# Kernel optimization log

Hardware: AMD Instinct MI355X
Metric: run time of the kernel (lower is better)

Reference implementation:

```python
import jax, jax.numpy as jnp
import numpy as np

NUM_HEADS = 16


def setup_inputs() -> dict:
    k0 = jax.random.key(0)
    ks = jax.random.split(k0, 5)
    T, S, N, E = 1024, 1024, 8, 1024
    query = jax.random.normal(ks[0], (T, N, E), dtype=jnp.float32)
    key_t = jax.random.normal(ks[1], (S, N, E), dtype=jnp.float32)
    value = jax.random.normal(ks[2], (S, N, E), dtype=jnp.float32)
    # xavier-uniform-like scale for in_proj (fan_in=fan_out-ish): gain*sqrt(6/(3E+E))
    lim_in = float(np.sqrt(6.0 / (3 * E + E)))
    in_proj_weight = jax.random.uniform(ks[3], (3 * E, E), dtype=jnp.float32, minval=-lim_in, maxval=lim_in)
    in_proj_bias = jnp.zeros((3 * E,), dtype=jnp.float32)
    lim_out = float(np.sqrt(1.0 / E))
    out_proj_weight = jax.random.uniform(ks[4], (E, E), dtype=jnp.float32, minval=-lim_out, maxval=lim_out)
    out_proj_bias = jnp.zeros((E,), dtype=jnp.float32)
    return {
        'query': query, 'key': key_t, 'value': value,
        'in_proj_weight': in_proj_weight, 'in_proj_bias': in_proj_bias,
        'out_proj_weight': out_proj_weight, 'out_proj_bias': out_proj_bias,
    }


def reference(query, key, value, in_proj_weight, in_proj_bias, out_proj_weight, out_proj_bias):
    # Faithful to the source: q,k,v ALL come from `query` via the 3E in-projection
    # (the torch code projects only `query` and chunks; key/value tensors unused).
    T, N, E = query.shape
    S = key.shape[0]  # must equal T for the reshape, as in the torch code
    H = NUM_HEADS
    D = E // H
    qkv = jnp.einsum('tne,fe->tnf', query, in_proj_weight) + in_proj_bias  # (T,N,3E)
    q, k, v = jnp.split(qkv, 3, axis=-1)
    q = q * (float(D) ** -0.5)
    # (T, N*H, D) -> (N*H, T, D)
    q = q.reshape(T, N * H, D).transpose(1, 0, 2)
    k = k.reshape(S, N * H, D).transpose(1, 0, 2)
    v = v.reshape(S, N * H, D).transpose(1, 0, 2)
    attn = jnp.einsum('btd,bsd->bts', q, k)          # (N*H, T, S)
    attn = jax.nn.softmax(attn, axis=-1)
    out = jnp.einsum('bts,bsd->btd', attn, v)        # (N*H, T, D)
    out = out.transpose(1, 0, 2).reshape(T, N, E)
    out = jnp.einsum('tne,fe->tnf', out, out_proj_weight) + out_proj_bias
    avg_weights = attn.reshape(N, H, T, S).mean(axis=1)  # (N, T, S)
    return out, avg_weights
```

## Files before the change

kernel.cpp:

```cpp
#include <hip/hip_runtime.h>


typedef __bf16 bf16x8 __attribute__((ext_vector_type(8)));
typedef float f32x4 __attribute__((ext_vector_type(4)));
typedef unsigned int u32;
typedef const __attribute__((address_space(1))) u32 gu32;
typedef __attribute__((address_space(3))) u32 lu32;

#define MFMA(a, b, c) __builtin_amdgcn_mfma_f32_16x16x32_bf16((a), (b), (c), 0, 0, 0)

#if __has_builtin(__builtin_amdgcn_exp2f)
#define EXP2(x) __builtin_amdgcn_exp2f(x)
#else
#define EXP2(x) exp2f(x)
#endif

__device__ __forceinline__ unsigned short f2bf(float x) {
    union { float f; unsigned u; } v; v.f = x;
    unsigned r = v.u + 0x7fffu + ((v.u >> 16) & 1u);
    return (unsigned short)(r >> 16);
}

__device__ __forceinline__ bf16x8 frag_ld(const unsigned short* p) {
    return __builtin_bit_cast(bf16x8, *(const uint4*)p);
}

template<int ROWS>
__device__ __forceinline__ void stageNx64(const unsigned short* g, int gs,
                                          unsigned short* lds, int wave, int lane) {
#pragma unroll
    for (int it = 0; it < ROWS / 32; it++) {
        int chunk = wave * (ROWS / 32) + it;
        int row = chunk * 8 + (lane >> 3);
        int cb = (lane & 7) ^ (row & 7);
        const unsigned short* gp = g + (size_t)row * gs + cb * 8;
        unsigned short* lp = lds + chunk * 512;
        __builtin_amdgcn_global_load_lds((gu32*)gp, (lu32*)lp, 16, 0, 0);
    }
}

__device__ __forceinline__ bf16x8 frag_sw(const unsigned short* lds, int row, int cb) {
    return frag_ld(lds + row * 64 + ((cb ^ (row & 7)) << 3));
}

__global__ void k_convert_all(const float* __restrict__ q, const float* __restrict__ wi,
                              const float* __restrict__ wo,
                              unsigned short* __restrict__ xq, unsigned short* __restrict__ xwi,
                              unsigned short* __restrict__ xwo) {
    int i = blockIdx.x * 256 + threadIdx.x;
    const float* src; unsigned short* dst; int off;
    if (i < 2097152)      { src = q;  dst = xq;  off = i; }
    else if (i < 2883584) { src = wi; dst = xwi; off = i - 2097152; }
    else                  { src = wo; dst = xwo; off = i - 2883584; }
    float4 v = ((const float4*)src)[off];
    ushort4 o;
    o.x = f2bf(v.x); o.y = f2bf(v.y); o.z = f2bf(v.z); o.w = f2bf(v.w);
    ((ushort4*)dst)[off] = o;
}

__global__ __launch_bounds__(256) void k_inproj(
    const unsigned short* __restrict__ A, const unsigned short* __restrict__ B,
    const float* __restrict__ bias,
    unsigned short* __restrict__ qbf, unsigned short* __restrict__ kbf,
    unsigned short* __restrict__ vTbf)
{
    __shared__ unsigned short As[128 * 64];
    __shared__ unsigned short Bs[128 * 64];
    const int tid = threadIdx.x;
    const int wave = tid >> 6, lane = tid & 63;
    const int quad = lane >> 4, l16 = lane & 15;
    const int wm = wave >> 1, wn = wave & 1;
    const int m0 = blockIdx.x * 128, n0 = blockIdx.y * 128;

    f32x4 acc[4][4];
#pragma unroll
    for (int i = 0; i < 4; i++)
#pragma unroll
        for (int j = 0; j < 4; j++) acc[i][j] = (f32x4){0.f, 0.f, 0.f, 0.f};

    for (int kt = 0; kt < 1024; kt += 64) {
        __syncthreads();
        stageNx64<128>(A + (size_t)m0 * 1024 + kt, 1024, As, wave, lane);
        stageNx64<128>(B + (size_t)n0 * 1024 + kt, 1024, Bs, wave, lane);
        __syncthreads();
#pragma unroll
        for (int kc = 0; kc < 2; kc++) {
            bf16x8 af[4], bfr[4];
#pragma unroll
            for (int i = 0; i < 4; i++) af[i]  = frag_sw(As, wm * 64 + i * 16 + l16, kc * 4 + quad);
#pragma unroll
            for (int j = 0; j < 4; j++) bfr[j] = frag_sw(Bs, wn * 64 + j * 16 + l16, kc * 4 + quad);
#pragma unroll
            for (int i = 0; i < 4; i++)
#pragma unroll
                for (int j = 0; j < 4; j++) acc[i][j] = MFMA(af[i], bfr[j], acc[i][j]);
        }
    }
    const float QSCALE = 0.125f * 1.4426950408889634f;
    const int c = n0 >> 10;
#pragma unroll
    for (int i = 0; i < 4; i++) {
#pragma unroll
        for (int j = 0; j < 4; j++) {
            int col = n0 + wn * 64 + j * 16 + l16;
            float bv = bias[col];
            int hd = col & 1023, h = hd >> 6, d = hd & 63;
#pragma unroll
            for (int r = 0; r < 4; r++) {
                int row = m0 + wm * 64 + i * 16 + quad * 4 + r;
                int t = row >> 3, n = row & 7;
                int b = n * 16 + h;
                float val = acc[i][j][r] + bv;
                if (c == 0)      qbf[(size_t)b * 65536 + t * 64 + d] = f2bf(val * QSCALE);
                else if (c == 1) kbf[(size_t)b * 65536 + t * 64 + d] = f2bf(val);
                else             vTbf[(size_t)b * 65536 + (size_t)d * 1024 + t] = f2bf(val);
            }
        }
    }
}

__global__ __launch_bounds__(256) void k_pv(
    const unsigned short* __restrict__ qbf, const unsigned short* __restrict__ kbf,
    const unsigned short* __restrict__ vTbf,
    float* __restrict__ il_g, unsigned short* __restrict__ Obf)
{
    __shared__ unsigned short Ks[64 * 64];
    __shared__ unsigned short Vs[64 * 64];
    __shared__ unsigned short Ps[128 * 64];
    const int tid = threadIdx.x;
    const int wave = tid >> 6, lane = tid & 63, quad = lane >> 4, l16 = lane & 15;
    const int blk = blockIdx.x;
    const int xcd = blk & 7, idx = blk >> 3;
    const int b = xcd * 16 + (idx >> 3);
    const int t0 = (idx & 7) * 128;
    const int n = b >> 4, h = b & 15;
    const size_t bb = (size_t)b * 65536;

    bf16x8 aq[2][2];
#pragma unroll
    for (int rf = 0; rf < 2; rf++)
#pragma unroll
        for (int kh = 0; kh < 2; kh++)
            aq[rf][kh] = frag_ld(&qbf[bb + (size_t)(t0 + wave * 32 + rf * 16 + l16) * 64 + kh * 32 + quad * 8]);

    float lsum[2][4];
    f32x4 o[2][4];
#pragma unroll
    for (int rf = 0; rf < 2; rf++)
#pragma unroll
        for (int r = 0; r < 4; r++) lsum[rf][r] = 0.f;
#pragma unroll
    for (int rf = 0; rf < 2; rf++)
#pragma unroll
        for (int df = 0; df < 4; df++) o[rf][df] = (f32x4){0.f, 0.f, 0.f, 0.f};

    for (int st = 0; st < 16; st++) {
        __syncthreads();
        stageNx64<64>(kbf + bb + (size_t)(st * 64) * 64, 64, Ks, wave, lane);
        stageNx64<64>(vTbf + bb + st * 64, 1024, Vs, wave, lane);
        __syncthreads();
#pragma unroll
        for (int cf = 0; cf < 4; cf++) {
            bf16x8 k0 = frag_sw(Ks, cf * 16 + l16, quad);
            bf16x8 k1 = frag_sw(Ks, cf * 16 + l16, 4 + quad);
#pragma unroll
            for (int rf = 0; rf < 2; rf++) {
                f32x4 z = (f32x4){0.f, 0.f, 0.f, 0.f};
                z = MFMA(aq[rf][0], k0, z);
                z = MFMA(aq[rf][1], k1, z);
#pragma unroll
                for (int r = 0; r < 4; r++) {
                    float p = EXP2(z[r]);
                    lsum[rf][r] += p;
                    int prow = wave * 32 + rf * 16 + quad * 4 + r;
                    int col = cf * 16 + l16;
                    Ps[prow * 64 + (((col >> 3) ^ (prow & 7)) << 3) + (col & 7)] = f2bf(p);
                }
            }
        }
#pragma unroll
        for (int kc = 0; kc < 2; kc++) {
            bf16x8 ap0 = frag_sw(Ps, wave * 32 + l16, kc * 4 + quad);
            bf16x8 ap1 = frag_sw(Ps, wave * 32 + 16 + l16, kc * 4 + quad);
#pragma unroll
            for (int df = 0; df < 4; df++) {
                bf16x8 bv = frag_sw(Vs, df * 16 + l16, kc * 4 + quad);
                o[0][df] = MFMA(ap0, bv, o[0][df]);
                o[1][df] = MFMA(ap1, bv, o[1][df]);
            }
        }
    }
#pragma unroll
    for (int rf = 0; rf < 2; rf++)
#pragma unroll
        for (int r = 0; r < 4; r++) {
            float s = lsum[rf][r];
            s += __shfl_xor(s, 1); s += __shfl_xor(s, 2);
            s += __shfl_xor(s, 4); s += __shfl_xor(s, 8);
            lsum[rf][r] = 1.0f / s;
        }
#pragma unroll
    for (int rf = 0; rf < 2; rf++)
#pragma unroll
        for (int df = 0; df < 4; df++)
#pragma unroll
            for (int r = 0; r < 4; r++) {
                int t = t0 + wave * 32 + rf * 16 + quad * 4 + r;
                Obf[(size_t)(t * 8 + n) * 1024 + h * 64 + df * 16 + l16] = f2bf(o[rf][df][r] * lsum[rf][r]);
            }
    if (l16 == 0) {
#pragma unroll
        for (int rf = 0; rf < 2; rf++)
#pragma unroll
            for (int r = 0; r < 4; r++)
                il_g[(size_t)b * 1024 + t0 + wave * 32 + rf * 16 + quad * 4 + r] = lsum[rf][r];
    }
}

__global__ __launch_bounds__(256) void k_avg(
    const unsigned short* __restrict__ qbf, const unsigned short* __restrict__ kbf,
    const float* __restrict__ il_g, float* __restrict__ avg)
{
    __shared__ unsigned short Qs[128 * 64];
    __shared__ unsigned short Ks[128 * 64];
    __shared__ float Is[16 * 128];
    const int tid = threadIdx.x;
    const int wave = tid >> 6, lane = tid & 63, quad = lane >> 4, l16 = lane & 15;
    const int wm = wave >> 1, wn = wave & 1;
    const int blk = blockIdx.x;
    const int n = blk & 7, idx = blk >> 3;
    const int s0 = (idx & 7) * 128, t0 = (idx >> 3) * 128;

    for (int i2 = tid; i2 < 2048; i2 += 256)
        Is[i2] = il_g[(size_t)(n * 16 + (i2 >> 7)) * 1024 + t0 + (i2 & 127)];

    f32x4 acc[4][4];
#pragma unroll
    for (int i = 0; i < 4; i++)
#pragma unroll
        for (int j = 0; j < 4; j++) acc[i][j] = (f32x4){0.f, 0.f, 0.f, 0.f};

    for (int h = 0; h < 16; h++) {
        const size_t bb = (size_t)(n * 16 + h) * 65536;
        __syncthreads();
        stageNx64<128>(qbf + bb + (size_t)t0 * 64, 64, Qs, wave, lane);
        stageNx64<128>(kbf + bb + (size_t)s0 * 64, 64, Ks, wave, lane);
        __syncthreads();
        bf16x8 af[4][2];
        float ir[4][4];
#pragma unroll
        for (int i = 0; i < 4; i++) {
            af[i][0] = frag_sw(Qs, wm * 64 + i * 16 + l16, quad);
            af[i][1] = frag_sw(Qs, wm * 64 + i * 16 + l16, 4 + quad);
#pragma unroll
            for (int r = 0; r < 4; r++) ir[i][r] = Is[h * 128 + wm * 64 + i * 16 + quad * 4 + r];
        }
#pragma unroll
        for (int j = 0; j < 4; j++) {
            bf16x8 b0 = frag_sw(Ks, wn * 64 + j * 16 + l16, quad);
            bf16x8 b1 = frag_sw(Ks, wn * 64 + j * 16 + l16, 4 + quad);
#pragma unroll
            for (int i = 0; i < 4; i++) {
                f32x4 z = (f32x4){0.f, 0.f, 0.f, 0.f};
                z = MFMA(af[i][0], b0, z);
                z = MFMA(af[i][1], b1, z);
#pragma unroll
                for (int r = 0; r < 4; r++)
                    acc[i][j][r] += EXP2(z[r]) * ir[i][r];
            }
        }
    }
#pragma unroll
    for (int i = 0; i < 4; i++)
#pragma unroll
        for (int j = 0; j < 4; j++)
#pragma unroll
            for (int r = 0; r < 4; r++) {
                int t = t0 + wm * 64 + i * 16 + quad * 4 + r;
                int s = s0 + wn * 64 + j * 16 + l16;
                avg[(size_t)n * 1048576 + (size_t)t * 1024 + s] = acc[i][j][r] * 0.0625f;
            }
}

__global__ __launch_bounds__(256) void k_outproj(
    const unsigned short* __restrict__ A, const unsigned short* __restrict__ B,
    const float* __restrict__ bias, float* __restrict__ out)
{
    __shared__ unsigned short As[128 * 64];
    __shared__ unsigned short Bs[128 * 64];
    const int tid = threadIdx.x;
    const int wave = tid >> 6, lane = tid & 63;
    const int quad = lane >> 4, l16 = lane & 15;
    const int wm = wave >> 1, wn = wave & 1;
    const int m0 = blockIdx.x * 128, n0 = blockIdx.y * 128;

    f32x4 acc[4][4];
#pragma unroll
    for (int i = 0; i < 4; i++)
#pragma unroll
        for (int j = 0; j < 4; j++) acc[i][j] = (f32x4){0.f, 0.f, 0.f, 0.f};

    for (int kt = 0; kt < 1024; kt += 64) {
        __syncthreads();
        stageNx64<128>(A + (size_t)m0 * 1024 + kt, 1024, As, wave, lane);
        stageNx64<128>(B + (size_t)n0 * 1024 + kt, 1024, Bs, wave, lane);
        __syncthreads();
#pragma unroll
        for (int kc = 0; kc < 2; kc++) {
            bf16x8 af[4], bfr[4];
#pragma unroll
            for (int i = 0; i < 4; i++) af[i]  = frag_sw(As, wm * 64 + i * 16 + l16, kc * 4 + quad);
#pragma unroll
            for (int j = 0; j < 4; j++) bfr[j] = frag_sw(Bs, wn * 64 + j * 16 + l16, kc * 4 + quad);
#pragma unroll
            for (int i = 0; i < 4; i++)
#pragma unroll
                for (int j = 0; j < 4; j++) acc[i][j] = MFMA(af[i], bfr[j], acc[i][j]);
        }
    }
#pragma unroll
    for (int i = 0; i < 4; i++)
#pragma unroll
        for (int j = 0; j < 4; j++) {
            int col = n0 + wn * 64 + j * 16 + l16;
            float bv = bias[col];
#pragma unroll
            for (int r = 0; r < 4; r++) {
                int row = m0 + wm * 64 + i * 16 + quad * 4 + r;
                out[(size_t)row * 1024 + col] = acc[i][j][r] + bv;
            }
        }
}

extern "C" void kernel_launch(void* const* d_in, const int* in_sizes, int n_in,
                              void* d_out, int out_size, void* d_ws, size_t ws_size,
                              hipStream_t stream)
{
    const float* query = (const float*)d_in[0];
    const float* w_in  = (const float*)d_in[3];
    const float* b_in  = (const float*)d_in[4];
    const float* w_out = (const float*)d_in[5];
    const float* b_out = (const float*)d_in[6];
    float* out = (float*)d_out;
    float* avg = out + 8388608;

    if (ws_size < ((size_t)73 << 20)) return;

    char* ws = (char*)d_ws;
    unsigned short* qbf  = (unsigned short*)(ws);
    unsigned short* kbf  = (unsigned short*)(ws + ((size_t)16 << 20));
    unsigned short* vTbf = (unsigned short*)(ws + ((size_t)32 << 20));
    unsigned short* xbf  = (unsigned short*)(ws + ((size_t)48 << 20));
    unsigned short* wibf = (unsigned short*)(ws + ((size_t)64 << 20));
    unsigned short* wobf = (unsigned short*)(ws + ((size_t)70 << 20));
    float* il_g = (float*)(ws + ((size_t)72 << 20));

    k_convert_all<<<12288, 256, 0, stream>>>(query, w_in, w_out, xbf, wibf, wobf);
    k_inproj<<<dim3(64, 24), 256, 0, stream>>>(xbf, wibf, b_in, qbf, kbf, vTbf);
    k_pv    <<<1024, 256, 0, stream>>>(qbf, kbf, vTbf, il_g, xbf);
    k_avg   <<<512, 256, 0, stream>>>(qbf, kbf, il_g, avg);
    k_outproj<<<dim3(64, 8), 256, 0, stream>>>(xbf, wobf, b_out, out);
}
```

Measured before the change: 357.4 us.

## Double-buffer LDS tiles in projection, PV and averaged-weight kernels

All four tiled kernels now hold two LDS buffers per operand. Each iteration starts staging the next tile while computing on the current one, and only one barrier remains per iteration instead of two. The aim is to hide global-to-LDS load latency behind the MFMA and exp work. The cost is double the LDS per block, which may lower occupancy, particularly for the 64KB GEMM and averaged-weight kernels.

```diff
diff --git a/kernel.cpp b/kernel.cpp
--- a/kernel.cpp
+++ b/kernel.cpp
@@ -64,13 +64,15 @@
     unsigned short* __restrict__ qbf, unsigned short* __restrict__ kbf,
     unsigned short* __restrict__ vTbf)
 {
-    __shared__ unsigned short As[128 * 64];
-    __shared__ unsigned short Bs[128 * 64];
+    __shared__ unsigned short As[2][128 * 64];
+    __shared__ unsigned short Bs[2][128 * 64];
     const int tid = threadIdx.x;
     const int wave = tid >> 6, lane = tid & 63;
     const int quad = lane >> 4, l16 = lane & 15;
     const int wm = wave >> 1, wn = wave & 1;
     const int m0 = blockIdx.x * 128, n0 = blockIdx.y * 128;
+    const unsigned short* Ab = A + (size_t)m0 * 1024;
+    const unsigned short* Bb = B + (size_t)n0 * 1024;
 
     f32x4 acc[4][4];
 #pragma unroll
@@ -78,23 +80,28 @@
 #pragma unroll
         for (int j = 0; j < 4; j++) acc[i][j] = (f32x4){0.f, 0.f, 0.f, 0.f};
 
-    for (int kt = 0; kt < 1024; kt += 64) {
-        __syncthreads();
-        stageNx64<128>(A + (size_t)m0 * 1024 + kt, 1024, As, wave, lane);
-        stageNx64<128>(B + (size_t)n0 * 1024 + kt, 1024, Bs, wave, lane);
-        __syncthreads();
+    stageNx64<128>(Ab, 1024, As[0], wave, lane);
+    stageNx64<128>(Bb, 1024, Bs[0], wave, lane);
+    __syncthreads();
+    for (int it = 0; it < 16; it++) {
+        const int cur = it & 1;
+        if (it < 15) {
+            stageNx64<128>(Ab + (it + 1) * 64, 1024, As[cur ^ 1], wave, lane);
+            stageNx64<128>(Bb + (it + 1) * 64, 1024, Bs[cur ^ 1], wave, lane);
+        }
 #pragma unroll
         for (int kc = 0; kc < 2; kc++) {
             bf16x8 af[4], bfr[4];
 #pragma unroll
-            for (int i = 0; i < 4; i++) af[i]  = frag_sw(As, wm * 64 + i * 16 + l16, kc * 4 + quad);
-#pragma unroll
-            for (int j = 0; j < 4; j++) bfr[j] = frag_sw(Bs, wn * 64 + j * 16 + l16, kc * 4 + quad);
+            for (int i = 0; i < 4; i++) af[i]  = frag_sw(As[cur], wm * 64 + i * 16 + l16, kc * 4 + quad);
+#pragma unroll
+            for (int j = 0; j < 4; j++) bfr[j] = frag_sw(Bs[cur], wn * 64 + j * 16 + l16, kc * 4 + quad);
 #pragma unroll
             for (int i = 0; i < 4; i++)
 #pragma unroll
                 for (int j = 0; j < 4; j++) acc[i][j] = MFMA(af[i], bfr[j], acc[i][j]);
         }
+        __syncthreads();
     }
     const float QSCALE = 0.125f * 1.4426950408889634f;
     const int c = n0 >> 10;
@@ -124,8 +131,8 @@
     const unsigned short* __restrict__ vTbf,
     float* __restrict__ il_g, unsigned short* __restrict__ Obf)
 {
-    __shared__ unsigned short Ks[64 * 64];
-    __shared__ unsigned short Vs[64 * 64];
+    __shared__ unsigned short Ks[2][64 * 64];
+    __shared__ unsigned short Vs[2][64 * 64];
     __shared__ unsigned short Ps[128 * 64];
     const int tid = threadIdx.x;
     const int wave = tid >> 6, lane = tid & 63, quad = lane >> 4, l16 = lane & 15;
@@ -154,15 +161,19 @@
 #pragma unroll
         for (int df = 0; df < 4; df++) o[rf][df] = (f32x4){0.f, 0.f, 0.f, 0.f};
 
+    stageNx64<64>(kbf + bb, 64, Ks[0], wave, lane);
+    stageNx64<64>(vTbf + bb, 1024, Vs[0], wave, lane);
+    __syncthreads();
     for (int st = 0; st < 16; st++) {
-        __syncthreads();
-        stageNx64<64>(kbf + bb + (size_t)(st * 64) * 64, 64, Ks, wave, lane);
-        stageNx64<64>(vTbf + bb + st * 64, 1024, Vs, wave, lane);
-        __syncthreads();
+        const int cur = st & 1;
+        if (st < 15) {
+            stageNx64<64>(kbf + bb + (size_t)((st + 1) * 64) * 64, 64, Ks[cur ^ 1], wave, lane);
+            stageNx64<64>(vTbf + bb + (st + 1) * 64, 1024, Vs[cur ^ 1], wave, lane);
+        }
 #pragma unroll
         for (int cf = 0; cf < 4; cf++) {
-            bf16x8 k0 = frag_sw(Ks, cf * 16 + l16, quad);
-            bf16x8 k1 = frag_sw(Ks, cf * 16 + l16, 4 + quad);
+            bf16x8 k0 = frag_sw(Ks[cur], cf * 16 + l16, quad);
+            bf16x8 k1 = frag_sw(Ks[cur], cf * 16 + l16, 4 + quad);
 #pragma unroll
             for (int rf = 0; rf < 2; rf++) {
                 f32x4 z = (f32x4){0.f, 0.f, 0.f, 0.f};
@@ -184,11 +195,12 @@
             bf16x8 ap1 = frag_sw(Ps, wave * 32 + 16 + l16, kc * 4 + quad);
 #pragma unroll
             for (int df = 0; df < 4; df++) {
-                bf16x8 bv = frag_sw(Vs, df * 16 + l16, kc * 4 + quad);
+                bf16x8 bv = frag_sw(Vs[cur], df * 16 + l16, kc * 4 + quad);
                 o[0][df] = MFMA(ap0, bv, o[0][df]);
                 o[1][df] = MFMA(ap1, bv, o[1][df]);
             }
         }
+        __syncthreads();
     }
 #pragma unroll
     for (int rf = 0; rf < 2; rf++)
@@ -221,8 +233,8 @@
     const unsigned short* __restrict__ qbf, const unsigned short* __restrict__ kbf,
     const float* __restrict__ il_g, float* __restrict__ avg)
 {
-    __shared__ unsigned short Qs[128 * 64];
-    __shared__ unsigned short Ks[128 * 64];
+    __shared__ unsigned short Qs[2][128 * 64];
+    __shared__ unsigned short Ks[2][128 * 64];
     __shared__ float Is[16 * 128];
     const int tid = threadIdx.x;
     const int wave = tid >> 6, lane = tid & 63, quad = lane >> 4, l16 = lane & 15;
@@ -240,25 +252,29 @@
 #pragma unroll
         for (int j = 0; j < 4; j++) acc[i][j] = (f32x4){0.f, 0.f, 0.f, 0.f};
 
+    stageNx64<128>(qbf + (size_t)(n * 16) * 65536 + (size_t)t0 * 64, 64, Qs[0], wave, lane);
+    stageNx64<128>(kbf + (size_t)(n * 16) * 65536 + (size_t)s0 * 64, 64, Ks[0], wave, lane);
+    __syncthreads();
     for (int h = 0; h < 16; h++) {
-        const size_t bb = (size_t)(n * 16 + h) * 65536;
-        __syncthreads();
-        stageNx64<128>(qbf + bb + (size_t)t0 * 64, 64, Qs, wave, lane);
-        stageNx64<128>(kbf + bb + (size_t)s0 * 64, 64, Ks, wave, lane);
-        __syncthreads();
+        const int cur = h & 1;
+        if (h < 15) {
+            const size_t bb1 = (size_t)(n * 16 + h + 1) * 65536;
+            stageNx64<128>(qbf + bb1 + (size_t)t0 * 64, 64, Qs[cur ^ 1], wave, lane);
+            stageNx64<128>(kbf + bb1 + (size_t)s0 * 64, 64, Ks[cur ^ 1], wave, lane);
+        }
         bf16x8 af[4][2];
         float ir[4][4];
 #pragma unroll
         for (int i = 0; i < 4; i++) {
-            af[i][0] = frag_sw(Qs, wm * 64 + i * 16 + l16, quad);
-            af[i][1] = frag_sw(Qs, wm * 64 + i * 16 + l16, 4 + quad);
+            af[i][0] = frag_sw(Qs[cur], wm * 64 + i * 16 + l16, quad);
+            af[i][1] = frag_sw(Qs[cur], wm * 64 + i * 16 + l16, 4 + quad);
 #pragma unroll
             for (int r = 0; r < 4; r++) ir[i][r] = Is[h * 128 + wm * 64 + i * 16 + quad * 4 + r];
         }
 #pragma unroll
         for (int j = 0; j < 4; j++) {
-            bf16x8 b0 = frag_sw(Ks, wn * 64 + j * 16 + l16, quad);
-            bf16x8 b1 = frag_sw(Ks, wn * 64 + j * 16 + l16, 4 + quad);
+            bf16x8 b0 = frag_sw(Ks[cur], wn * 64 + j * 16 + l16, quad);
+            bf16x8 b1 = frag_sw(Ks[cur], wn * 64 + j * 16 + l16, 4 + quad);
 #pragma unroll
             for (int i = 0; i < 4; i++) {
                 f32x4 z = (f32x4){0.f, 0.f, 0.f, 0.f};
@@ -269,6 +285,7 @@
                     acc[i][j][r] += EXP2(z[r]) * ir[i][r];
             }
         }
+        __syncthreads();
     }
 #pragma unroll
     for (int i = 0; i < 4; i++)
@@ -286,13 +303,15 @@
     const unsigned short* __restrict__ A, const unsigned short* __restrict__ B,
     const float* __restrict__ bias, float* __restrict__ out)
 {
-    __shared__ unsigned short As[128 * 64];
-    __shared__ unsigned short Bs[128 * 64];
+    __shared__ unsigned short As[2][128 * 64];
+    __shared__ unsigned short Bs[2][128 * 64];
     const int tid = threadIdx.x;
     const int wave = tid >> 6, lane = tid & 63;
     const int quad = lane >> 4, l16 = lane & 15;
     const int wm = wave >> 1, wn = wave & 1;
     const int m0 = blockIdx.x * 128, n0 = blockIdx.y * 128;
+    const unsigned short* Ab = A + (size_t)m0 * 1024;
+    const unsigned short* Bb = B + (size_t)n0 * 1024;
 
     f32x4 acc[4][4];
 #pragma unroll
@@ -300,23 +319,28 @@
 #pragma unroll
         for (int j = 0; j < 4; j++) acc[i][j] = (f32x4){0.f, 0.f, 0.f, 0.f};
 
-    for (int kt = 0; kt < 1024; kt += 64) {
-        __syncthreads();
-        stageNx64<128>(A + (size_t)m0 * 1024 + kt, 1024, As, wave, lane);
-        stageNx64<128>(B + (size_t)n0 * 1024 + kt, 1024, Bs, wave, lane);
-        __syncthreads();
+    stageNx64<128>(Ab, 1024, As[0], wave, lane);
+    stageNx64<128>(Bb, 1024, Bs[0], wave, lane);
+    __syncthreads();
+    for (int it = 0; it < 16; it++) {
+        const int cur = it & 1;
+        if (it < 15) {
+            stageNx64<128>(Ab + (it + 1) * 64, 1024, As[cur ^ 1], wave, lane);
+            stageNx64<128>(Bb + (it + 1) * 64, 1024, Bs[cur ^ 1], wave, lane);
+        }
 #pragma unroll
         for (int kc = 0; kc < 2; kc++) {
             bf16x8 af[4], bfr[4];
 #pragma unroll
-            for (int i = 0; i < 4; i++) af[i]  = frag_sw(As, wm * 64 + i * 16 + l16, kc * 4 + quad);
-#pragma unroll
-            for (int j = 0; j < 4; j++) bfr[j] = frag_sw(Bs, wn * 64 + j * 16 + l16, kc * 4 + quad);
+            for (int i = 0; i < 4; i++) af[i]  = frag_sw(As[cur], wm * 64 + i * 16 + l16, kc * 4 + quad);
+#pragma unroll
+            for (int j = 0; j < 4; j++) bfr[j] = frag_sw(Bs[cur], wn * 64 + j * 16 + l16, kc * 4 + quad);
 #pragma unroll
             for (int i = 0; i < 4; i++)
 #pragma unroll
                 for (int j = 0; j < 4; j++) acc[i][j] = MFMA(af[i], bfr[j], acc[i][j]);
         }
+        __syncthreads();
     }
 #pragma unroll
     for (int i = 0; i < 4; i++)
```

Measured after the change: 355.9 us. Within noise of the previous version (-0.4%).
